# Optimization experiments

Measured on AMD Instinct MI355X. Metric: run time of the kernel, lower is better.

## Reference

```python
import jax, jax.numpy as jnp
import numpy as np

B, S, D_IN = 16, 512, 768
HID, OUT = 64, 12
NEG = 1e12


def setup_inputs() -> dict:
    key = jax.random.key(0)
    k1, k2, k3 = jax.random.split(key, 3)
    x = jax.random.normal(k1, (B, S, D_IN), dtype=jnp.float32)
    mask = jnp.ones((B, S), dtype=jnp.float32)
    W = jax.random.normal(k2, (D_IN, HID * OUT * 2), dtype=jnp.float32) * 0.02
    b = jax.random.normal(k3, (HID * OUT * 2,), dtype=jnp.float32) * 0.02
    return {"x": x, "mask": mask, "W": W, "b": b}


def reference(x, mask, W, b):
    Bb, Ss, _ = x.shape
    h, out = HID, OUT
    # QKV-style projection, split into `out` heads of 2h each
    proj = (x @ W + b).reshape(Bb, Ss, out, 2 * h)  # [b, s, out, 2h]
    qw, kw = proj[..., :h], proj[..., h:]           # [b, s, out, h]

    # Sinusoidal position embedding (merge='zero'): interleaved sin/cos
    pos_ids = jnp.arange(Ss, dtype=x.dtype)
    inv_freq = jnp.power(10000.0, -2.0 * jnp.arange(h // 2, dtype=x.dtype) / h)
    ang = pos_ids[:, None] * inv_freq               # [s, h/2]
    sin, cos = jnp.sin(ang), jnp.cos(ang)
    # torch: pos[..., None, 1::2].repeat(1,1,1,2) -> TILED (not interleaved)
    cos_pos = jnp.concatenate([cos, cos], axis=-1)[None, :, None, :]  # [1, s, 1, h]
    sin_pos = jnp.concatenate([sin, sin], axis=-1)[None, :, None, :]

    def rope(w):
        # stack([-w_odd, w_even], -1).reshape -> interleaved rotation partner
        w2 = jnp.stack([-w[..., 1::2], w[..., ::2]], axis=-1).reshape(w.shape)
        return w * cos_pos + w2 * sin_pos

    qw = rope(qw)
    kw = rope(kw)

    logits = jnp.einsum('bmhd,bnhd->bhmn', qw, kw)  # [b, out, s, s]

    pad = mask[:, None, None, :]                    # broadcast over [b, out, s, s]
    logits = logits * pad - (1.0 - pad) * NEG

    tril = jnp.tril(jnp.ones((Ss, Ss), dtype=logits.dtype), -1)
    logits = logits - tril * NEG

    return logits / (h ** 0.5)
```

## Files before the change

kernel.cpp:

```cpp
#include <hip/hip_runtime.h>
#include <stdint.h>

#define DIN   768
#define NPROJ 1536
#define SEQ   512
#define NHEAD 12
#define NBATCH 16
#define NEGV  1000000000000.0f

typedef short bf16x8 __attribute__((ext_vector_type(8)));
typedef float f32x4  __attribute__((ext_vector_type(4)));
typedef unsigned short u16x8 __attribute__((ext_vector_type(8)));

__device__ __forceinline__ unsigned short f2bf(float f) {
    union { float f; unsigned int u; } v; v.f = f;
    return (unsigned short)((v.u + 0x7FFFu + ((v.u >> 16) & 1u)) >> 16);
}
__device__ __forceinline__ float bf2f(unsigned short u) {
    union { unsigned int u; float f; } v; v.u = ((unsigned int)u) << 16;
    return v.f;
}

__device__ __forceinline__ void gl_lds16(const unsigned short* g, unsigned short* l) {
    __builtin_amdgcn_global_load_lds(
        (const __attribute__((address_space(1))) unsigned int*)(uintptr_t)g,
        (__attribute__((address_space(3))) unsigned int*)(uintptr_t)l,
        16, 0, 0);
}

__device__ __forceinline__ void stage128x64(const unsigned short* __restrict__ g,
                                            int gstride, unsigned short* lds,
                                            int w, int lane) {
#pragma unroll
    for (int t = 0; t < 4; t++) {
        int lr = w * 32 + t * 8 + (lane >> 3);
        int c16 = (lane & 7) ^ (lr & 7);
        gl_lds16(g + (size_t)lr * gstride + c16 * 8,
                 lds + (w * 32 + t * 8) * 64);
    }
}
__device__ __forceinline__ int swz(int row, int cg) {
    return row * 64 + ((cg ^ (row & 7)) << 3);
}

__global__ __launch_bounds__(256) void k_prep(const float* __restrict__ X,
                                              unsigned short* __restrict__ Xb,
                                              const float* __restrict__ W,
                                              unsigned short* __restrict__ Wt,
                                              float* __restrict__ trig) {
    __shared__ unsigned short T[64][72];
    const int bid = blockIdx.x, tid = threadIdx.x;
    if (bid < 288) {
        int n0 = (bid % 24) * 64, k0 = (bid / 24) * 64;
#pragma unroll
        for (int it = 0; it < 4; it++) {
            int c = tid + it * 256;
            int kl = c >> 4, nl = (c & 15) * 4;
            float4 v = *(const float4*)&W[(size_t)(k0 + kl) * NPROJ + n0 + nl];
            T[nl + 0][kl] = f2bf(v.x);
            T[nl + 1][kl] = f2bf(v.y);
            T[nl + 2][kl] = f2bf(v.z);
            T[nl + 3][kl] = f2bf(v.w);
        }
        __syncthreads();
#pragma unroll
        for (int it = 0; it < 2; it++) {
            int c = tid + it * 256;
            int nl = c >> 3, kb = (c & 7) * 8;
            *(int4*)&Wt[(size_t)(n0 + nl) * DIN + k0 + kb] = *(int4*)&T[nl][kb];
        }
        return;
    }
    if (bid < 352) {
        int gi = (bid - 288) * 256 + tid;
        int ss = gi >> 5, j = gi & 31;
        const float C = 0.41524101186092034f;
        float cs, sn;
        sincosf((float)ss * exp2f(-(float)j * C), &sn, &cs);
        trig[2 * gi]     = cs;
        trig[2 * gi + 1] = sn;
        return;
    }
    int i = ((bid - 352) * 256 + tid) * 4;
    float4 v = *(const float4*)&X[i];
    short4 s;
    s.x = (short)f2bf(v.x); s.y = (short)f2bf(v.y);
    s.z = (short)f2bf(v.z); s.w = (short)f2bf(v.w);
    *(short4*)&Xb[i] = s;
}

template <bool PRE>
__global__ __launch_bounds__(256) void k_gemm(const float* __restrict__ X,
                                              const unsigned short* __restrict__ Xb,
                                              const unsigned short* __restrict__ Wt,
                                              const float* __restrict__ bias,
                                              const float* __restrict__ trig,
                                              unsigned short* __restrict__ P) {
    __shared__ unsigned short smem[17408];
    unsigned short* sA = smem;
    unsigned short* sB = smem + 8192;
    const int tid = threadIdx.x;
    const int m0 = blockIdx.y * 128, n0 = blockIdx.x * 128;
    const int lane = tid & 63, w = tid >> 6;
    const int q = lane >> 4, r = lane & 15;
    const int wm = w >> 1, wn = w & 1;
    f32x4 acc[4][4];
#pragma unroll
    for (int i = 0; i < 4; i++)
#pragma unroll
        for (int j = 0; j < 4; j++) acc[i][j] = (f32x4){0.f, 0.f, 0.f, 0.f};

    const unsigned short* Ag = Xb + (size_t)m0 * DIN;
    const unsigned short* Bg = Wt + (size_t)n0 * DIN;

    for (int k0 = 0; k0 < DIN; k0 += 64) {
        __syncthreads();
        if (PRE) {
            stage128x64(Ag + k0, DIN, sA, w, lane);
        } else {
#pragma unroll
            for (int it = 0; it < 4; it++) {
                int c = tid + it * 256;
                int row = c >> 3, c16 = c & 7;
                const float* xp = &X[(size_t)(m0 + row) * DIN + k0 + c16 * 8];
                float4 v0 = *(const float4*)xp;
                float4 v1 = *(const float4*)(xp + 4);
                u16x8 sv;
                sv[0] = f2bf(v0.x); sv[1] = f2bf(v0.y);
                sv[2] = f2bf(v0.z); sv[3] = f2bf(v0.w);
                sv[4] = f2bf(v1.x); sv[5] = f2bf(v1.y);
                sv[6] = f2bf(v1.z); sv[7] = f2bf(v1.w);
                *(u16x8*)&sA[swz(row, c16)] = sv;
            }
        }
        stage128x64(Bg + k0, DIN, sB, w, lane);
        __syncthreads();
#pragma unroll
        for (int kk = 0; kk < 64; kk += 32) {
            const int cg = (kk >> 3) + q;
            bf16x8 af[4], bfr[4];
#pragma unroll
            for (int t = 0; t < 4; t++)
                af[t] = *(const bf16x8*)&sA[swz(wm * 64 + t * 16 + r, cg)];
#pragma unroll
            for (int t = 0; t < 4; t++)
                bfr[t] = *(const bf16x8*)&sB[swz(wn * 64 + t * 16 + r, cg)];
#pragma unroll
            for (int tm = 0; tm < 4; tm++)
#pragma unroll
                for (int tn = 0; tn < 4; tn++)
                    acc[tm][tn] = __builtin_amdgcn_mfma_f32_16x16x32_bf16(
                        af[tm], bfr[tn], acc[tm][tn], 0, 0, 0);
        }
    }
    float bb[4];
#pragma unroll
    for (int tn = 0; tn < 4; tn++) bb[tn] = bias[n0 + wn * 64 + tn * 16 + r];
    __syncthreads();
    unsigned short* sT = smem;
#pragma unroll
    for (int tm = 0; tm < 4; tm++) {
        int rowb = wm * 64 + tm * 16 + q * 4;
#pragma unroll
        for (int tn = 0; tn < 4; tn++) {
            int col = wn * 64 + tn * 16 + r;
#pragma unroll
            for (int i = 0; i < 4; i++)
                sT[(rowb + i) * 136 + col] = f2bf(acc[tm][tn][i] + bb[tn]);
        }
    }
    __syncthreads();
#pragma unroll
    for (int it = 0; it < 8; it++) {
        int c = tid + it * 256;
        int row = c >> 4, colb = (c & 15) * 8;
        int m = m0 + row;
        int s = m & (SEQ - 1);
        int base = colb & 31;
        union { int4 v; unsigned short u[8]; } pk;
        pk.v = *(int4*)&sT[row * 136 + colb];
        float wv[8];
#pragma unroll
        for (int j = 0; j < 8; j++) wv[j] = bf2f(pk.u[j]);
        const float* tp = &trig[2 * (s * 32 + base)];
#pragma unroll
        for (int p = 0; p < 4; p++) {
            float4 tt = *(const float4*)&tp[4 * p];
            float oe = wv[2 * p] * tt.x - wv[2 * p + 1] * tt.y;
            float oo = wv[2 * p + 1] * tt.z + wv[2 * p] * tt.w;
            pk.u[2 * p]     = f2bf(oe);
            pk.u[2 * p + 1] = f2bf(oo);
        }
        *(int4*)&P[(size_t)m * NPROJ + n0 + colb] = pk.v;
    }
}

__global__ __launch_bounds__(256, 3) void k_attn(const unsigned short* __restrict__ P,
                                                 const float* __restrict__ mask,
                                                 float* __restrict__ out) {
    __shared__ unsigned short sQ[8192];
    __shared__ unsigned short sK[2][8192];
    const int tid = threadIdx.x;
    int lid = blockIdx.x + 4 * (blockIdx.y + NHEAD * blockIdx.z);
    lid = (lid & 7) * 96 + (lid >> 3);
    const int mt = lid & 3;
    const int h  = (lid >> 2) % NHEAD;
    const int b  = lid / (4 * NHEAD);
    const int lane = tid & 63, w = tid >> 6;
    const int q = lane >> 4, r = lane & 15;
    const int wm = w >> 1, wn = w & 1;
    const size_t obase = ((size_t)((b * NHEAD + h) * SEQ)) * SEQ;

    const unsigned short* Pbh = P + (size_t)b * SEQ * NPROJ + h * 128;
    stage128x64(Pbh + (size_t)(mt * 128) * NPROJ, NPROJ, sQ, w, lane);
    stage128x64(Pbh + (size_t)(mt * 128) * NPROJ + 64, NPROJ, sK[0], w, lane);

    int cur = 0;
    for (int nt = mt; nt < 4; nt++) {
        __syncthreads();
        if (nt + 1 < 4)
            stage128x64(Pbh + (size_t)((nt + 1) * 128) * NPROJ + 64, NPROJ,
                        sK[cur ^ 1], w, lane);
        const unsigned short* sk = sK[cur];

        f32x4 acc[4][4];
#pragma unroll
        for (int i = 0; i < 4; i++)
#pragma unroll
            for (int j = 0; j < 4; j++) acc[i][j] = (f32x4){0.f, 0.f, 0.f, 0.f};
#pragma unroll
        for (int x2 = 0; x2 < 2; x2++) {
            const int cg = x2 * 4 + q;
            bf16x8 af[4], bfr[4];
#pragma unroll
            for (int t = 0; t < 4; t++)
                af[t] = *(const bf16x8*)&sQ[swz(wm * 64 + t * 16 + r, cg)];
#pragma unroll
            for (int t = 0; t < 4; t++)
                bfr[t] = *(const bf16x8*)&sk[swz(wn * 64 + t * 16 + r, cg)];
#pragma unroll
            for (int tn = 0; tn < 4; tn++)
#pragma unroll
                for (int tm = 0; tm < 4; tm++)
                    acc[tn][tm] = __builtin_amdgcn_mfma_f32_16x16x32_bf16(
                        bfr[tn], af[tm], acc[tn][tm], 0, 0, 0);
        }
        const int ncol0 = nt * 128;
        f32x4 mk4[4];
#pragma unroll
        for (int tn = 0; tn < 4; tn++)
            mk4[tn] = *(const f32x4*)&mask[b * SEQ + ncol0 + wn * 64 + tn * 16 + q * 4];
#pragma unroll
        for (int tm = 0; tm < 4; tm++) {
            const int m = mt * 128 + wm * 64 + tm * 16 + r;
            float* orow = out + obase + (size_t)m * SEQ;
#pragma unroll
            for (int tn = 0; tn < 4; tn++) {
                const int nb = ncol0 + wn * 64 + tn * 16 + q * 4;
                f32x4 o;
#pragma unroll
                for (int j = 0; j < 4; j++)
                    o[j] = (acc[tn][tm][j] * mk4[tn][j]
                            - (1.f - mk4[tn][j]) * NEGV
                            - ((nb + j) < m ? NEGV : 0.f)) * 0.125f;
                __builtin_nontemporal_store(o, (f32x4*)(orow + nb));
            }
        }
        cur ^= 1;
    }
    for (int nt = 0; nt < mt; nt++) {
#pragma unroll
        for (int it = 0; it < 16; it++) {
            int c = tid + it * 256;
            int rl = c >> 5, cb = (c & 31) * 4;
            int m = mt * 128 + rl, n = nt * 128 + cb;
            f32x4 mk = *(const f32x4*)&mask[b * SEQ + n];
            f32x4 o;
#pragma unroll
            for (int j = 0; j < 4; j++)
                o[j] = (-(1.f - mk[j]) * NEGV - NEGV) * 0.125f;
            __builtin_nontemporal_store(o, (f32x4*)&out[obase + (size_t)m * SEQ + n]);
        }
    }
}

extern "C" void kernel_launch(void* const* d_in, const int* in_sizes, int n_in,
                              void* d_out, int out_size, void* d_ws, size_t ws_size,
                              hipStream_t stream) {
    const float* x    = (const float*)d_in[0];
    const float* mask = (const float*)d_in[1];
    const float* W    = (const float*)d_in[2];
    const float* bias = (const float*)d_in[3];
    float* out = (float*)d_out;

    const size_t wtN   = (size_t)NPROJ * DIN;
    const size_t pN    = (size_t)NBATCH * SEQ * NPROJ;
    const size_t xN    = (size_t)NBATCH * SEQ * DIN;
    const size_t trigN = (size_t)SEQ * 32 * 2;
    unsigned short* Wt = (unsigned short*)d_ws;
    unsigned short* P  = Wt + wtN;
    float* trig        = (float*)(P + pN);
    unsigned short* Xb = (unsigned short*)(trig + trigN);
    const bool pre = ws_size >= (wtN + pN + xN) * sizeof(unsigned short)
                               + trigN * sizeof(float);

    const int xblocks = (int)(xN / 1024);
    k_prep<<<pre ? (352 + xblocks) : 352, 256, 0, stream>>>(x, Xb, W, Wt, trig);
    if (pre) {
        k_gemm<true><<<dim3(NPROJ / 128, (NBATCH * SEQ) / 128), 256, 0, stream>>>(
            x, Xb, Wt, bias, trig, P);
    } else {
        k_gemm<false><<<dim3(NPROJ / 128, (NBATCH * SEQ) / 128), 256, 0, stream>>>(
            x, nullptr, Wt, bias, trig, P);
    }
    k_attn<<<dim3(4, NHEAD, NBATCH), 256, 0, stream>>>(P, mask, out);
}
```

Measured before the change: 304.7 us.

## Retile attention kernel to 32-row blocks with full K in LDS and staged output

The logits kernel now launches one block per 32 query rows per (batch, head), giving 3072 small blocks instead of 768 blocks of 128 rows. Each block loads all 512 keys into LDS once and keeps Q fragments in registers. Each wave computes a 16-column strip for both 16-row tiles and skips fully masked column tiles. Results are written to LDS first, then stored as fully contiguous rows to global memory. The aim is better load balance across the causal triangle and more coalesced stores. The cost is that every block reloads all of K, LDS use grows to 64KB, and occupancy drops.

```diff
diff --git a/kernel.cpp b/kernel.cpp
--- a/kernel.cpp
+++ b/kernel.cpp
@@ -195,92 +195,99 @@
     }
 }
 
-__global__ __launch_bounds__(256, 3) void k_attn(const unsigned short* __restrict__ P,
+__global__ __launch_bounds__(256, 2) void k_attn(const unsigned short* __restrict__ P,
                                                  const float* __restrict__ mask,
                                                  float* __restrict__ out) {
-    __shared__ unsigned short sQ[8192];
-    __shared__ unsigned short sK[2][8192];
+    __shared__ __attribute__((aligned(16))) unsigned short smem[32768];
     const int tid = threadIdx.x;
-    int lid = blockIdx.x + 4 * (blockIdx.y + NHEAD * blockIdx.z);
-    lid = (lid & 7) * 96 + (lid >> 3);
-    const int mt = lid & 3;
-    const int h  = (lid >> 2) % NHEAD;
-    const int b  = lid / (4 * NHEAD);
-    const int lane = tid & 63, w = tid >> 6;
+    const int bi = blockIdx.x;
+    const int x  = bi & 7, s = bi >> 3;
+    const int g  = x + 8 * (s >> 4);
+    const int rb = s & 15;
+    const int b  = g / NHEAD, h = g % NHEAD;
+    const int lane = tid & 63, wn = tid >> 6;
     const int q = lane >> 4, r = lane & 15;
-    const int wm = w >> 1, wn = w & 1;
+    const int w = wn;
     const size_t obase = ((size_t)((b * NHEAD + h) * SEQ)) * SEQ;
-
-    const unsigned short* Pbh = P + (size_t)b * SEQ * NPROJ + h * 128;
-    stage128x64(Pbh + (size_t)(mt * 128) * NPROJ, NPROJ, sQ, w, lane);
-    stage128x64(Pbh + (size_t)(mt * 128) * NPROJ + 64, NPROJ, sK[0], w, lane);
-
-    int cur = 0;
-    for (int nt = mt; nt < 4; nt++) {
-        __syncthreads();
-        if (nt + 1 < 4)
-            stage128x64(Pbh + (size_t)((nt + 1) * 128) * NPROJ + 64, NPROJ,
-                        sK[cur ^ 1], w, lane);
-        const unsigned short* sk = sK[cur];
-
-        f32x4 acc[4][4];
-#pragma unroll
-        for (int i = 0; i < 4; i++)
-#pragma unroll
-            for (int j = 0; j < 4; j++) acc[i][j] = (f32x4){0.f, 0.f, 0.f, 0.f};
-#pragma unroll
-        for (int x2 = 0; x2 < 2; x2++) {
-            const int cg = x2 * 4 + q;
-            bf16x8 af[4], bfr[4];
-#pragma unroll
-            for (int t = 0; t < 4; t++)
-                af[t] = *(const bf16x8*)&sQ[swz(wm * 64 + t * 16 + r, cg)];
-#pragma unroll
-            for (int t = 0; t < 4; t++)
-                bfr[t] = *(const bf16x8*)&sk[swz(wn * 64 + t * 16 + r, cg)];
-#pragma unroll
-            for (int tn = 0; tn < 4; tn++)
-#pragma unroll
-                for (int tm = 0; tm < 4; tm++)
-                    acc[tn][tm] = __builtin_amdgcn_mfma_f32_16x16x32_bf16(
-                        bfr[tn], af[tm], acc[tn][tm], 0, 0, 0);
-        }
-        const int ncol0 = nt * 128;
-        f32x4 mk4[4];
-#pragma unroll
-        for (int tn = 0; tn < 4; tn++)
-            mk4[tn] = *(const f32x4*)&mask[b * SEQ + ncol0 + wn * 64 + tn * 16 + q * 4];
-#pragma unroll
-        for (int tm = 0; tm < 4; tm++) {
-            const int m = mt * 128 + wm * 64 + tm * 16 + r;
-            float* orow = out + obase + (size_t)m * SEQ;
-#pragma unroll
-            for (int tn = 0; tn < 4; tn++) {
-                const int nb = ncol0 + wn * 64 + tn * 16 + q * 4;
-                f32x4 o;
+    const int m0 = rb * 32;
+
+    const unsigned short* Pk = P + (size_t)b * SEQ * NPROJ + h * 128 + 64;
+#pragma unroll
+    for (int c = 0; c < 4; c++)
+        stage128x64(Pk + (size_t)(c * 128) * NPROJ, NPROJ, smem + c * 128 * 64, w, lane);
+
+    const unsigned short* Pq = P + (size_t)b * SEQ * NPROJ + h * 128;
+    bf16x8 qf[2][2];
+#pragma unroll
+    for (int rt = 0; rt < 2; rt++)
+#pragma unroll
+        for (int x2 = 0; x2 < 2; x2++)
+            qf[rt][x2] = *(const bf16x8*)
+                &Pq[(size_t)(m0 + rt * 16 + r) * NPROJ + x2 * 32 + q * 8];
+
+    f32x4 mk4[8];
+#pragma unroll
+    for (int t = 0; t < 8; t++)
+        mk4[t] = *(const f32x4*)&mask[b * SEQ + (wn * 8 + t) * 16 + q * 4];
+
+    f32x4 acc[8][2];
+#pragma unroll
+    for (int t = 0; t < 8; t++) {
+        acc[t][0] = (f32x4){0.f, 0.f, 0.f, 0.f};
+        acc[t][1] = (f32x4){0.f, 0.f, 0.f, 0.f};
+    }
+
+    __syncthreads();
+
+#pragma unroll
+    for (int t = 0; t < 8; t++) {
+        const int ct = wn * 8 + t;
+        if (ct >= 2 * rb) {
+            bf16x8 kf[2];
+#pragma unroll
+            for (int x2 = 0; x2 < 2; x2++)
+                kf[x2] = *(const bf16x8*)&smem[swz(ct * 16 + r, x2 * 4 + q)];
+#pragma unroll
+            for (int x2 = 0; x2 < 2; x2++) {
+                acc[t][0] = __builtin_amdgcn_mfma_f32_16x16x32_bf16(
+                    kf[x2], qf[0][x2], acc[t][0], 0, 0, 0);
+                acc[t][1] = __builtin_amdgcn_mfma_f32_16x16x32_bf16(
+                    kf[x2], qf[1][x2], acc[t][1], 0, 0, 0);
+            }
+        }
+    }
+    __syncthreads();
+
+    float* sOut = (float*)smem;
+#pragma unroll
+    for (int rt = 0; rt < 2; rt++) {
+        const int m = m0 + rt * 16 + r;
+#pragma unroll
+        for (int t = 0; t < 8; t++) {
+            const int ct = wn * 8 + t;
+            const int nb = ct * 16 + q * 4;
+            f32x4 o;
+            if (ct >= 2 * rb) {
 #pragma unroll
                 for (int j = 0; j < 4; j++)
-                    o[j] = (acc[tn][tm][j] * mk4[tn][j]
-                            - (1.f - mk4[tn][j]) * NEGV
+                    o[j] = (acc[t][rt][j] * mk4[t][j]
+                            - (1.f - mk4[t][j]) * NEGV
                             - ((nb + j) < m ? NEGV : 0.f)) * 0.125f;
-                __builtin_nontemporal_store(o, (f32x4*)(orow + nb));
+            } else {
+#pragma unroll
+                for (int j = 0; j < 4; j++)
+                    o[j] = (-(1.f - mk4[t][j]) * NEGV - NEGV) * 0.125f;
             }
-        }
-        cur ^= 1;
-    }
-    for (int nt = 0; nt < mt; nt++) {
-#pragma unroll
-        for (int it = 0; it < 16; it++) {
-            int c = tid + it * 256;
-            int rl = c >> 5, cb = (c & 31) * 4;
-            int m = mt * 128 + rl, n = nt * 128 + cb;
-            f32x4 mk = *(const f32x4*)&mask[b * SEQ + n];
-            f32x4 o;
-#pragma unroll
-            for (int j = 0; j < 4; j++)
-                o[j] = (-(1.f - mk[j]) * NEGV - NEGV) * 0.125f;
-            __builtin_nontemporal_store(o, (f32x4*)&out[obase + (size_t)m * SEQ + n]);
-        }
+            *(f32x4*)&sOut[(rt * 16 + r) * 512 + nb] = o;
+        }
+    }
+    __syncthreads();
+    float* od = out + obase + (size_t)m0 * SEQ;
+#pragma unroll
+    for (int it = 0; it < 16; it++) {
+        const int c = tid + it * 256;
+        f32x4 v = *(const f32x4*)&sOut[c * 4];
+        __builtin_nontemporal_store(v, (f32x4*)&od[c * 4]);
     }
 }
 
@@ -313,5 +320,5 @@
         k_gemm<false><<<dim3(NPROJ / 128, (NBATCH * SEQ) / 128), 256, 0, stream>>>(
             x, nullptr, Wt, bias, trig, P);
     }
-    k_attn<<<dim3(4, NHEAD, NBATCH), 256, 0, stream>>>(P, mask, out);
-}
+    k_attn<<<dim3(NBATCH * NHEAD * (SEQ / 32)), 256, 0, stream>>>(P, mask, out);
+}
```

Result: faster. 277.3 us (-9.0%).
